# Performance work log

Measured on AMD Instinct MI355X. Metric: run time of the kernel, lower is better.

The kernel has to match this reference:

```python
import jax, jax.numpy as jnp
import numpy as np

B = 512          # batch
IN_UNITS = 8     # primary capsule dim
IN_CH = 1152     # number of primary capsules
NUM_UNITS = 10   # output capsules (classes)
UNIT_SIZE = 16   # output capsule dim
BETA = 1.45      # squash beta: 1.45 - 0.22*(ep_iter/total) with ep_iter = n_iter = 0
NUM_ROUTING = 3


def setup_inputs() -> dict:
    key = jax.random.key(0)
    k1, k2 = jax.random.split(key)
    x = jax.random.normal(k1, (B, IN_UNITS, IN_CH), dtype=jnp.float32)
    # W parameter: torch shape (1, in_channels, num_units, unit_size, in_units); drop leading 1
    W = jax.random.normal(k2, (IN_CH, NUM_UNITS, UNIT_SIZE, IN_UNITS), dtype=jnp.float32)
    return {"x": x, "W": W}


def _squash(s):
    # s: (B, num_units, unit_size). Torch squash sums dim=2 of (B,1,nu,us,1),
    # which is the num_units axis (axis=1 here). Faithful to source.
    mag_sq = jnp.sum(s * s, axis=1, keepdims=True)          # (B,1,us)
    mag = jnp.sqrt(mag_sq)
    return mag_sq / (BETA + mag_sq) * (s / mag)


def reference(x, W):
    # u_hat[b,i,j,u] = sum_k W[i,j,u,k] * x[b,k,i]
    u_hat = jnp.einsum('ijuk,bki->biju', W, x)               # (B, IN_CH, NUM_UNITS, UNIT_SIZE)
    b_ij = jnp.zeros((IN_CH, NUM_UNITS), dtype=x.dtype)
    v = None
    for _ in range(NUM_ROUTING):
        c = jax.nn.softmax(b_ij, axis=0)                     # softmax over in_channels (dim=1 in torch)
        s = jnp.einsum('ij,biju->bju', c, u_hat)             # (B, NUM_UNITS, UNIT_SIZE)
        v = _squash(s)
        # b update: agreement <u_hat, v>, averaged over batch
        b_ij = jnp.einsum('biju,bju->ij', u_hat, v) / u_hat.shape[0]
    # rearrange 'b c (g h) w -> b c g (h w)' with g=4, w=1 -> reshape (B, nu, 4, us//4)
    return v.reshape(v.shape[0], NUM_UNITS, 4, UNIT_SIZE // 4)
```

## Files before the change

### kernel.cpp

```cpp
#include <hip/hip_runtime.h>
#include <hip/hip_bf16.h>
#include <math.h>

#define B    512
#define INU  8
#define IC   1152
#define NU   10
#define US   16
#define JU   160
#define KI   9216
#define BETAC 1.45f
#define NSPLIT 32
#define KC 288

typedef __attribute__((ext_vector_type(8))) __bf16 bf16x8;
typedef __attribute__((ext_vector_type(4))) float floatx4;

static __device__ __forceinline__ unsigned short f2bf(float f) {
  unsigned u = __builtin_bit_cast(unsigned, f);
  u = (u + 0x7fffu + ((u >> 16) & 1u)) >> 16;
  return (unsigned short)u;
}
static __device__ __forceinline__ float bf2f(unsigned short h) {
  return __builtin_bit_cast(float, ((unsigned)h) << 16);
}
static __device__ __forceinline__ uint4 scale8(uint4 wv, float4 cA, float4 cB) {
  union { uint4 u; unsigned short s[8]; } in;
  in.u = wv;
  union { uint4 u; __hip_bfloat162 h[4]; } o;
  o.h[0] = __float22bfloat162_rn(make_float2(bf2f(in.s[0]) * cA.x, bf2f(in.s[1]) * cA.y));
  o.h[1] = __float22bfloat162_rn(make_float2(bf2f(in.s[2]) * cA.z, bf2f(in.s[3]) * cA.w));
  o.h[2] = __float22bfloat162_rn(make_float2(bf2f(in.s[4]) * cB.x, bf2f(in.s[5]) * cB.y));
  o.h[3] = __float22bfloat162_rn(make_float2(bf2f(in.s[6]) * cB.z, bf2f(in.s[7]) * cB.w));
  return o.u;
}

__global__ __launch_bounds__(256) void prep_kernel(
    const float* __restrict__ x, const float* __restrict__ W,
    unsigned short* __restrict__ xb, unsigned short* __restrict__ xT,
    unsigned short* __restrict__ Wt, float* __restrict__ Wr,
    float* __restrict__ cT) {
  __shared__ float ts[32 * 322];
  int id = blockIdx.x;
  int t = threadIdx.x;
  if (id < 1152) {
    int k0 = (id % 144) * 64;
    int b0 = (id / 144) * 64;
#pragma unroll
    for (int r = 0; r < 16; ++r) {
      int idx = t + 256 * r;
      int br = idx >> 6, kc = idx & 63;
      float v = x[(size_t)(b0 + br) * KI + k0 + kc];
      ts[br * 65 + kc] = v;
      xb[(size_t)(b0 + br) * KI + k0 + kc] = f2bf(v);
    }
    __syncthreads();
#pragma unroll
    for (int r = 0; r < 8; ++r) {
      int idx = t + 256 * r;
      int kr = idx >> 5, bc = (idx & 31) * 2;
      unsigned lo = f2bf(ts[bc * 65 + kr]);
      unsigned hi = f2bf(ts[(bc + 1) * 65 + kr]);
      *(unsigned*)&xT[(size_t)(k0 + kr) * B + b0 + bc] = lo | (hi << 16);
    }
  } else {
    int wid = id - 1152;
    int i0 = (wid >> 2) * 32;
    int c0 = (wid & 3) * 320;
#pragma unroll
    for (int r = 0; r < 20; ++r) {
      int q = t + 256 * r;
      int il = q / 160, c = (q - il * 160) * 2;
      *(float2*)&ts[il * 322 + c] =
          *(const float2*)&W[(size_t)(i0 + il) * 1280 + c0 + c];
    }
    __syncthreads();
    {
      int il2 = (t & 15) * 2;
      for (int p = (t >> 4); p < 320; p += 16) {
        int c = c0 + p;
        int ju = c >> 3, k = c & 7;
        unsigned lo = f2bf(ts[il2 * 322 + p]);
        unsigned hi = f2bf(ts[(il2 + 1) * 322 + p]);
        *(unsigned*)&Wt[(size_t)ju * KI + k * IC + i0 + il2] = lo | (hi << 16);
      }
    }
    int ju0 = c0 >> 3;
    for (int q = t; q < 8 * 32 * 40; q += 256) {
      int k = q / 1280;
      int il = (q / 40) & 31;
      int jl = q - (q / 40) * 40;
      Wr[((size_t)k * IC + i0 + il) * JU + ju0 + jl] = ts[il * 322 + jl * 8 + k];
    }
    if (id == 1152) {
      for (int q = t; q < IC * NU; q += 256) cT[q] = 1.0f / (float)IC;
    }
  }
}

__global__ __launch_bounds__(256) void s_gemm_mfma(
    const unsigned short* __restrict__ xb, const unsigned short* __restrict__ Wt,
    const float* __restrict__ cT, float* __restrict__ sp) {
  int b0 = blockIdx.x * 64;
  int kbase = blockIdx.y * KC;
  int i0 = kbase % IC;
  int t = threadIdx.x;
  int w = t >> 6, lane = t & 63, col = lane & 15, quad = lane >> 4;
  __shared__ unsigned short xs[64 * 40];
  __shared__ unsigned short ms[160 * 40];
  __shared__ float cs[NU * KC];

  int xrow = t >> 2, xc = (t & 3) * 8;
  int mrow0 = t >> 2, mrow1 = (t + 256) >> 2, mrow2 = (t + 512) >> 2;
  int mc = (t & 3) * 8;
  int j0 = mrow0 >> 4, j1 = mrow1 >> 4, j2 = mrow2 >> 4;

  for (int ch = t; ch < NU * KC; ch += 256) {
    int j = ch / KC;
    cs[ch] = cT[j * IC + i0 + (ch - j * KC)];
  }
  uint4 xv, m0, m1, m2;
  auto prefetch = [&](int k0) {
    xv = *(const uint4*)&xb[(size_t)(b0 + xrow) * KI + k0 + xc];
    m0 = *(const uint4*)&Wt[(size_t)mrow0 * KI + k0 + mc];
    m1 = *(const uint4*)&Wt[(size_t)mrow1 * KI + k0 + mc];
    if (t < 128) m2 = *(const uint4*)&Wt[(size_t)mrow2 * KI + k0 + mc];
  };
  auto commit = [&](int off) {
    *(uint4*)&xs[xrow * 40 + xc] = xv;
    float4 a0 = *(const float4*)&cs[j0 * KC + off + mc];
    float4 a1 = *(const float4*)&cs[j0 * KC + off + mc + 4];
    *(uint4*)&ms[mrow0 * 40 + mc] = scale8(m0, a0, a1);
    float4 b0c = *(const float4*)&cs[j1 * KC + off + mc];
    float4 b1c = *(const float4*)&cs[j1 * KC + off + mc + 4];
    *(uint4*)&ms[mrow1 * 40 + mc] = scale8(m1, b0c, b1c);
    if (t < 128) {
      float4 d0 = *(const float4*)&cs[j2 * KC + off + mc];
      float4 d1 = *(const float4*)&cs[j2 * KC + off + mc + 4];
      *(uint4*)&ms[mrow2 * 40 + mc] = scale8(m2, d0, d1);
    }
  };
  floatx4 acc[10];
#pragma unroll
  for (int jt = 0; jt < 10; ++jt) acc[jt] = (floatx4){0.f, 0.f, 0.f, 0.f};
  prefetch(kbase);
  __syncthreads();
  const int nsteps = KC >> 5;
  for (int s = 0; s < nsteps; ++s) {
    commit(s * 32);
    __syncthreads();
    if (s + 1 < nsteps) prefetch(kbase + (s + 1) * 32);
    bf16x8 a = *(bf16x8*)&xs[(w * 16 + col) * 40 + quad * 8];
#pragma unroll
    for (int jt = 0; jt < 10; ++jt) {
      bf16x8 bb = *(bf16x8*)&ms[(jt * 16 + col) * 40 + quad * 8];
      acc[jt] = __builtin_amdgcn_mfma_f32_16x16x32_bf16(a, bb, acc[jt], 0, 0, 0);
    }
    __syncthreads();
  }
#pragma unroll
  for (int jt = 0; jt < 10; ++jt)
#pragma unroll
    for (int r = 0; r < 4; ++r) {
      int b = b0 + w * 16 + quad * 4 + r;
      sp[((size_t)blockIdx.y * B + b) * JU + jt * 16 + col] = acc[jt][r];
    }
}

__global__ __launch_bounds__(192) void squash_kernel(
    const float* __restrict__ sp, unsigned short* __restrict__ vT,
    float* __restrict__ out) {
  int b = blockIdx.x;
  int t = threadIdx.x;
  __shared__ float sv[JU];
  __shared__ float fac[US];
  float s = 0.0f;
  if (t < JU) {
#pragma unroll
    for (int k = 0; k < NSPLIT; ++k) s += sp[((size_t)k * B + b) * JU + t];
    sv[t] = s;
  }
  __syncthreads();
  if (t < US) {
    float m = 0.0f;
#pragma unroll
    for (int j = 0; j < NU; ++j) {
      float q = sv[j * US + t];
      m += q * q;
    }
    fac[t] = sqrtf(m) / (BETAC + m);
  }
  __syncthreads();
  if (t < JU) {
    float val = s * fac[t & 15];
    vT[(size_t)t * B + b] = f2bf(val);
    if (out) out[(size_t)b * JU + t] = val;
  }
}

__global__ __launch_bounds__(256) void b_update_mfma(
    const unsigned short* __restrict__ xT, const unsigned short* __restrict__ vT,
    const float* __restrict__ Wr, float* __restrict__ bp) {
  int k = blockIdx.x / 18;
  int i0 = (blockIdx.x - k * 18) * 64;
  int bs = blockIdx.y;
  size_t ki0 = (size_t)k * IC + i0;
  int t = threadIdx.x;
  int w = t >> 6, lane = t & 63, col = lane & 15, quad = lane >> 4;
  __shared__ unsigned short xs[64 * 40];
  __shared__ unsigned short vs[160 * 40];
  int xrow = t >> 2, xc = (t & 3) * 8;
  int mrow0 = t >> 2, mrow1 = (t + 256) >> 2, mrow2 = (t + 512) >> 2;
  int mc = (t & 3) * 8;
  uint4 xv, m0, m1, m2;
  auto prefetch = [&](int c0) {
    xv = *(const uint4*)&xT[(ki0 + xrow) * B + c0 + xc];
    m0 = *(const uint4*)&vT[(size_t)mrow0 * B + c0 + mc];
    m1 = *(const uint4*)&vT[(size_t)mrow1 * B + c0 + mc];
    if (t < 128) m2 = *(const uint4*)&vT[(size_t)mrow2 * B + c0 + mc];
  };
  auto commit = [&]() {
    *(uint4*)&xs[xrow * 40 + xc] = xv;
    *(uint4*)&vs[mrow0 * 40 + mc] = m0;
    *(uint4*)&vs[mrow1 * 40 + mc] = m1;
    if (t < 128) *(uint4*)&vs[mrow2 * 40 + mc] = m2;
  };
  floatx4 acc[10];
#pragma unroll
  for (int jt = 0; jt < 10; ++jt) acc[jt] = (floatx4){0.f, 0.f, 0.f, 0.f};
  prefetch(bs * 256);
  for (int s = 0; s < 8; ++s) {
    commit();
    __syncthreads();
    if (s < 7) prefetch(bs * 256 + (s + 1) * 32);
    bf16x8 a = *(bf16x8*)&xs[(w * 16 + col) * 40 + quad * 8];
#pragma unroll
    for (int jt = 0; jt < 10; ++jt) {
      bf16x8 bb = *(bf16x8*)&vs[(jt * 16 + col) * 40 + quad * 8];
      acc[jt] = __builtin_amdgcn_mfma_f32_16x16x32_bf16(a, bb, acc[jt], 0, 0, 0);
    }
    __syncthreads();
  }
  int p = k * 2 + bs;
#pragma unroll
  for (int jt = 0; jt < 10; ++jt) {
#pragma unroll
    for (int r = 0; r < 4; ++r) {
      int i = i0 + w * 16 + quad * 4 + r;
      float wv = Wr[((size_t)k * IC + i) * JU + jt * 16 + col];
      float pr = wv * acc[jt][r];
      pr += __shfl_xor(pr, 1);
      pr += __shfl_xor(pr, 2);
      pr += __shfl_xor(pr, 4);
      pr += __shfl_xor(pr, 8);
      if (col == 0)
        bp[(size_t)p * (IC * NU) + jt * IC + i] = pr * (1.0f / (float)B);
    }
  }
}

__global__ __launch_bounds__(256) void softmax_c_kernel(
    const float* __restrict__ bp, float* __restrict__ cT) {
  int j = blockIdx.x;
  int t = threadIdx.x;
  __shared__ float bsum[IC];
  __shared__ float red[256];
  for (int i = t; i < IC; i += 256) {
    float s = 0.0f;
#pragma unroll
    for (int p = 0; p < 16; ++p) s += bp[(size_t)p * (IC * NU) + j * IC + i];
    bsum[i] = s;
  }
  __syncthreads();
  float m = -1e30f;
  for (int i = t; i < IC; i += 256) m = fmaxf(m, bsum[i]);
  red[t] = m;
  __syncthreads();
  for (int o = 128; o > 0; o >>= 1) {
    if (t < o) red[t] = fmaxf(red[t], red[t + o]);
    __syncthreads();
  }
  float mx = red[0];
  __syncthreads();
  float sm = 0.0f;
  for (int i = t; i < IC; i += 256) {
    float e = __expf(bsum[i] - mx);
    bsum[i] = e;
    sm += e;
  }
  red[t] = sm;
  __syncthreads();
  for (int o = 128; o > 0; o >>= 1) {
    if (t < o) red[t] += red[t + o];
    __syncthreads();
  }
  float inv = 1.0f / red[0];
  for (int i = t; i < IC; i += 256) cT[(size_t)j * IC + i] = bsum[i] * inv;
}

extern "C" void kernel_launch(void* const* d_in, const int* in_sizes, int n_in,
                              void* d_out, int out_size, void* d_ws,
                              size_t ws_size, hipStream_t stream) {
  const float* x = (const float*)d_in[0];
  const float* W = (const float*)d_in[1];
  float* out = (float*)d_out;

  char* pws = (char*)d_ws;
  float* cT = (float*)pws;                     pws += (size_t)NU * IC * 4;
  float* bp = (float*)pws;                     pws += (size_t)16 * IC * NU * 4;
  float* sp = (float*)pws;                     pws += (size_t)NSPLIT * B * JU * 4;
  float* Wr = (float*)pws;                     pws += (size_t)KI * JU * 4;
  unsigned short* xb = (unsigned short*)pws;   pws += (size_t)B * KI * 2;
  unsigned short* xT = (unsigned short*)pws;   pws += (size_t)KI * B * 2;
  unsigned short* Wt = (unsigned short*)pws;   pws += (size_t)JU * KI * 2;
  unsigned short* vT = (unsigned short*)pws;

  prep_kernel<<<1152 + 144, 256, 0, stream>>>(x, W, xb, xT, Wt, Wr, cT);

  for (int it = 0; it < 3; ++it) {
    s_gemm_mfma<<<dim3(8, NSPLIT), 256, 0, stream>>>(xb, Wt, cT, sp);
    squash_kernel<<<B, 192, 0, stream>>>(sp, vT, (it == 2) ? out : nullptr);
    if (it < 2) {
      b_update_mfma<<<dim3(144, 2), 256, 0, stream>>>(xT, vT, Wr, bp);
      softmax_c_kernel<<<NU, 256, 0, stream>>>(bp, cT);
    }
  }
}
```

Baseline: 175.9 us.

## Pre-scale W by routing coefficients in softmax kernel and double-buffer GEMM LDS

The softmax kernel now writes a bf16 copy of W already scaled by the routing coefficients (Wc), launched over 160 blocks. The s-GEMM therefore no longer loads coefficients into shared memory or scales its tiles. prep initialises Wc with the uniform 1/IC scaling in place of a cT buffer. Both MFMA GEMMs also switch to double-buffered LDS with one barrier per step instead of two. This costs an extra bf16 W buffer and a full pass over W per routing iteration, and the scale is applied to an already-rounded bf16 W, so the value is rounded twice.

```diff
diff --git a/kernel.cpp b/kernel.cpp
--- a/kernel.cpp
+++ b/kernel.cpp
@@ -38,8 +38,8 @@
 __global__ __launch_bounds__(256) void prep_kernel(
     const float* __restrict__ x, const float* __restrict__ W,
     unsigned short* __restrict__ xb, unsigned short* __restrict__ xT,
-    unsigned short* __restrict__ Wt, float* __restrict__ Wr,
-    float* __restrict__ cT) {
+    unsigned short* __restrict__ Wt, unsigned short* __restrict__ Wc,
+    float* __restrict__ Wr) {
   __shared__ float ts[32 * 322];
   int id = blockIdx.x;
   int t = threadIdx.x;
@@ -76,6 +76,7 @@
     }
     __syncthreads();
     {
+      const float cinv = 1.0f / (float)IC;
       int il2 = (t & 15) * 2;
       for (int p = (t >> 4); p < 320; p += 16) {
         int c = c0 + p;
@@ -83,6 +84,9 @@
         unsigned lo = f2bf(ts[il2 * 322 + p]);
         unsigned hi = f2bf(ts[(il2 + 1) * 322 + p]);
         *(unsigned*)&Wt[(size_t)ju * KI + k * IC + i0 + il2] = lo | (hi << 16);
+        unsigned lo2 = f2bf(bf2f((unsigned short)lo) * cinv);
+        unsigned hi2 = f2bf(bf2f((unsigned short)hi) * cinv);
+        *(unsigned*)&Wc[(size_t)ju * KI + k * IC + i0 + il2] = lo2 | (hi2 << 16);
       }
     }
     int ju0 = c0 >> 3;
@@ -92,71 +96,53 @@
       int jl = q - (q / 40) * 40;
       Wr[((size_t)k * IC + i0 + il) * JU + ju0 + jl] = ts[il * 322 + jl * 8 + k];
     }
-    if (id == 1152) {
-      for (int q = t; q < IC * NU; q += 256) cT[q] = 1.0f / (float)IC;
-    }
   }
 }
 
 __global__ __launch_bounds__(256) void s_gemm_mfma(
-    const unsigned short* __restrict__ xb, const unsigned short* __restrict__ Wt,
-    const float* __restrict__ cT, float* __restrict__ sp) {
+    const unsigned short* __restrict__ xb, const unsigned short* __restrict__ Wc,
+    float* __restrict__ sp) {
   int b0 = blockIdx.x * 64;
   int kbase = blockIdx.y * KC;
-  int i0 = kbase % IC;
   int t = threadIdx.x;
   int w = t >> 6, lane = t & 63, col = lane & 15, quad = lane >> 4;
-  __shared__ unsigned short xs[64 * 40];
-  __shared__ unsigned short ms[160 * 40];
-  __shared__ float cs[NU * KC];
+  __shared__ unsigned short xs[2][64 * 40];
+  __shared__ unsigned short ms[2][160 * 40];
 
   int xrow = t >> 2, xc = (t & 3) * 8;
   int mrow0 = t >> 2, mrow1 = (t + 256) >> 2, mrow2 = (t + 512) >> 2;
   int mc = (t & 3) * 8;
-  int j0 = mrow0 >> 4, j1 = mrow1 >> 4, j2 = mrow2 >> 4;
-
-  for (int ch = t; ch < NU * KC; ch += 256) {
-    int j = ch / KC;
-    cs[ch] = cT[j * IC + i0 + (ch - j * KC)];
-  }
+
   uint4 xv, m0, m1, m2;
   auto prefetch = [&](int k0) {
     xv = *(const uint4*)&xb[(size_t)(b0 + xrow) * KI + k0 + xc];
-    m0 = *(const uint4*)&Wt[(size_t)mrow0 * KI + k0 + mc];
-    m1 = *(const uint4*)&Wt[(size_t)mrow1 * KI + k0 + mc];
-    if (t < 128) m2 = *(const uint4*)&Wt[(size_t)mrow2 * KI + k0 + mc];
+    m0 = *(const uint4*)&Wc[(size_t)mrow0 * KI + k0 + mc];
+    m1 = *(const uint4*)&Wc[(size_t)mrow1 * KI + k0 + mc];
+    if (t < 128) m2 = *(const uint4*)&Wc[(size_t)mrow2 * KI + k0 + mc];
   };
-  auto commit = [&](int off) {
-    *(uint4*)&xs[xrow * 40 + xc] = xv;
-    float4 a0 = *(const float4*)&cs[j0 * KC + off + mc];
-    float4 a1 = *(const float4*)&cs[j0 * KC + off + mc + 4];
-    *(uint4*)&ms[mrow0 * 40 + mc] = scale8(m0, a0, a1);
-    float4 b0c = *(const float4*)&cs[j1 * KC + off + mc];
-    float4 b1c = *(const float4*)&cs[j1 * KC + off + mc + 4];
-    *(uint4*)&ms[mrow1 * 40 + mc] = scale8(m1, b0c, b1c);
-    if (t < 128) {
-      float4 d0 = *(const float4*)&cs[j2 * KC + off + mc];
-      float4 d1 = *(const float4*)&cs[j2 * KC + off + mc + 4];
-      *(uint4*)&ms[mrow2 * 40 + mc] = scale8(m2, d0, d1);
-    }
+  auto commit = [&](int pb) {
+    *(uint4*)&xs[pb][xrow * 40 + xc] = xv;
+    *(uint4*)&ms[pb][mrow0 * 40 + mc] = m0;
+    *(uint4*)&ms[pb][mrow1 * 40 + mc] = m1;
+    if (t < 128) *(uint4*)&ms[pb][mrow2 * 40 + mc] = m2;
   };
   floatx4 acc[10];
 #pragma unroll
   for (int jt = 0; jt < 10; ++jt) acc[jt] = (floatx4){0.f, 0.f, 0.f, 0.f};
+  const int nsteps = KC >> 5;
   prefetch(kbase);
-  __syncthreads();
-  const int nsteps = KC >> 5;
+  commit(0);
+  prefetch(kbase + 32);
   for (int s = 0; s < nsteps; ++s) {
-    commit(s * 32);
-    __syncthreads();
-    if (s + 1 < nsteps) prefetch(kbase + (s + 1) * 32);
-    bf16x8 a = *(bf16x8*)&xs[(w * 16 + col) * 40 + quad * 8];
+    __syncthreads();
+    if (s + 1 < nsteps) commit((s + 1) & 1);
+    if (s + 2 < nsteps) prefetch(kbase + (s + 2) * 32);
+    bf16x8 a = *(bf16x8*)&xs[s & 1][(w * 16 + col) * 40 + quad * 8];
 #pragma unroll
     for (int jt = 0; jt < 10; ++jt) {
-      bf16x8 bb = *(bf16x8*)&ms[(jt * 16 + col) * 40 + quad * 8];
+      bf16x8 bb = *(bf16x8*)&ms[s & 1][(jt * 16 + col) * 40 + quad * 8];
       acc[jt] = __builtin_amdgcn_mfma_f32_16x16x32_bf16(a, bb, acc[jt], 0, 0, 0);
     }
-    __syncthreads();
   }
 #pragma unroll
   for (int jt = 0; jt < 10; ++jt)
@@ -207,8 +193,8 @@
   size_t ki0 = (size_t)k * IC + i0;
   int t = threadIdx.x;
   int w = t >> 6, lane = t & 63, col = lane & 15, quad = lane >> 4;
-  __shared__ unsigned short xs[64 * 40];
-  __shared__ unsigned short vs[160 * 40];
+  __shared__ unsigned short xs[2][64 * 40];
+  __shared__ unsigned short vs[2][160 * 40];
   int xrow = t >> 2, xc = (t & 3) * 8;
   int mrow0 = t >> 2, mrow1 = (t + 256) >> 2, mrow2 = (t + 512) >> 2;
   int mc = (t & 3) * 8;
@@ -219,27 +205,28 @@
     m1 = *(const uint4*)&vT[(size_t)mrow1 * B + c0 + mc];
     if (t < 128) m2 = *(const uint4*)&vT[(size_t)mrow2 * B + c0 + mc];
   };
-  auto commit = [&]() {
-    *(uint4*)&xs[xrow * 40 + xc] = xv;
-    *(uint4*)&vs[mrow0 * 40 + mc] = m0;
-    *(uint4*)&vs[mrow1 * 40 + mc] = m1;
-    if (t < 128) *(uint4*)&vs[mrow2 * 40 + mc] = m2;
+  auto commit = [&](int pb) {
+    *(uint4*)&xs[pb][xrow * 40 + xc] = xv;
+    *(uint4*)&vs[pb][mrow0 * 40 + mc] = m0;
+    *(uint4*)&vs[pb][mrow1 * 40 + mc] = m1;
+    if (t < 128) *(uint4*)&vs[pb][mrow2 * 40 + mc] = m2;
   };
   floatx4 acc[10];
 #pragma unroll
   for (int jt = 0; jt < 10; ++jt) acc[jt] = (floatx4){0.f, 0.f, 0.f, 0.f};
   prefetch(bs * 256);
+  commit(0);
+  prefetch(bs * 256 + 32);
   for (int s = 0; s < 8; ++s) {
-    commit();
-    __syncthreads();
-    if (s < 7) prefetch(bs * 256 + (s + 1) * 32);
-    bf16x8 a = *(bf16x8*)&xs[(w * 16 + col) * 40 + quad * 8];
+    __syncthreads();
+    if (s + 1 < 8) commit((s + 1) & 1);
+    if (s + 2 < 8) prefetch(bs * 256 + (s + 2) * 32);
+    bf16x8 a = *(bf16x8*)&xs[s & 1][(w * 16 + col) * 40 + quad * 8];
 #pragma unroll
     for (int jt = 0; jt < 10; ++jt) {
-      bf16x8 bb = *(bf16x8*)&vs[(jt * 16 + col) * 40 + quad * 8];
+      bf16x8 bb = *(bf16x8*)&vs[s & 1][(jt * 16 + col) * 40 + quad * 8];
       acc[jt] = __builtin_amdgcn_mfma_f32_16x16x32_bf16(a, bb, acc[jt], 0, 0, 0);
     }
-    __syncthreads();
   }
   int p = k * 2 + bs;
 #pragma unroll
@@ -259,21 +246,23 @@
   }
 }
 
-__global__ __launch_bounds__(256) void softmax_c_kernel(
-    const float* __restrict__ bp, float* __restrict__ cT) {
-  int j = blockIdx.x;
-  int t = threadIdx.x;
-  __shared__ float bsum[IC];
+__global__ __launch_bounds__(256) void softmax_scale_kernel(
+    const float* __restrict__ bp, const unsigned short* __restrict__ Wt,
+    unsigned short* __restrict__ Wc) {
+  int ju = blockIdx.x;
+  int j = ju >> 4;
+  int t = threadIdx.x;
+  __shared__ float c[IC];
   __shared__ float red[256];
   for (int i = t; i < IC; i += 256) {
     float s = 0.0f;
 #pragma unroll
     for (int p = 0; p < 16; ++p) s += bp[(size_t)p * (IC * NU) + j * IC + i];
-    bsum[i] = s;
+    c[i] = s;
   }
   __syncthreads();
   float m = -1e30f;
-  for (int i = t; i < IC; i += 256) m = fmaxf(m, bsum[i]);
+  for (int i = t; i < IC; i += 256) m = fmaxf(m, c[i]);
   red[t] = m;
   __syncthreads();
   for (int o = 128; o > 0; o >>= 1) {
@@ -284,8 +273,8 @@
   __syncthreads();
   float sm = 0.0f;
   for (int i = t; i < IC; i += 256) {
-    float e = __expf(bsum[i] - mx);
-    bsum[i] = e;
+    float e = __expf(c[i] - mx);
+    c[i] = e;
     sm += e;
   }
   red[t] = sm;
@@ -295,7 +284,14 @@
     __syncthreads();
   }
   float inv = 1.0f / red[0];
-  for (int i = t; i < IC; i += 256) cT[(size_t)j * IC + i] = bsum[i] * inv;
+  for (int q = t; q < KI / 8; q += 256) {
+    int ki = q * 8;
+    int i = ki % IC;
+    uint4 wv = *(const uint4*)&Wt[(size_t)ju * KI + ki];
+    float4 cA = make_float4(c[i] * inv, c[i + 1] * inv, c[i + 2] * inv, c[i + 3] * inv);
+    float4 cB = make_float4(c[i + 4] * inv, c[i + 5] * inv, c[i + 6] * inv, c[i + 7] * inv);
+    *(uint4*)&Wc[(size_t)ju * KI + ki] = scale8(wv, cA, cB);
+  }
 }
 
 extern "C" void kernel_launch(void* const* d_in, const int* in_sizes, int n_in,
@@ -306,23 +302,23 @@
   float* out = (float*)d_out;
 
   char* pws = (char*)d_ws;
-  float* cT = (float*)pws;                     pws += (size_t)NU * IC * 4;
   float* bp = (float*)pws;                     pws += (size_t)16 * IC * NU * 4;
   float* sp = (float*)pws;                     pws += (size_t)NSPLIT * B * JU * 4;
   float* Wr = (float*)pws;                     pws += (size_t)KI * JU * 4;
   unsigned short* xb = (unsigned short*)pws;   pws += (size_t)B * KI * 2;
   unsigned short* xT = (unsigned short*)pws;   pws += (size_t)KI * B * 2;
   unsigned short* Wt = (unsigned short*)pws;   pws += (size_t)JU * KI * 2;
+  unsigned short* Wc = (unsigned short*)pws;   pws += (size_t)JU * KI * 2;
   unsigned short* vT = (unsigned short*)pws;
 
-  prep_kernel<<<1152 + 144, 256, 0, stream>>>(x, W, xb, xT, Wt, Wr, cT);
+  prep_kernel<<<1152 + 144, 256, 0, stream>>>(x, W, xb, xT, Wt, Wc, Wr);
 
   for (int it = 0; it < 3; ++it) {
-    s_gemm_mfma<<<dim3(8, NSPLIT), 256, 0, stream>>>(xb, Wt, cT, sp);
+    s_gemm_mfma<<<dim3(8, NSPLIT), 256, 0, stream>>>(xb, Wc, sp);
     squash_kernel<<<B, 192, 0, stream>>>(sp, vT, (it == 2) ? out : nullptr);
     if (it < 2) {
       b_update_mfma<<<dim3(144, 2), 256, 0, stream>>>(xT, vT, Wr, bp);
-      softmax_c_kernel<<<NU, 256, 0, stream>>>(bp, cT);
-    }
-  }
-}
+      softmax_scale_kernel<<<160, 256, 0, stream>>>(bp, Wt, Wc);
+    }
+  }
+}
```

New measurement: 171.9 us. 1.02x faster.
